# Optimization experiments

Measured on AMD Instinct MI355X. Metric: run time of the kernel, lower is better.

The kernel has to match this reference:

```python
import math
import jax, jax.numpy as jnp
import numpy as np

D_MODEL = 1024
N_HEADS = 16


def setup_inputs() -> dict:
    key = jax.random.key(0)
    ks = jax.random.split(key, 5)
    B, S, D = 4, 2048, D_MODEL
    std = math.sqrt(2.0 / (D + D))
    x = jax.random.normal(ks[0], (B, S, D), dtype=jnp.float32)
    wq = jax.random.normal(ks[1], (D, D), dtype=jnp.float32) * std
    wk = jax.random.normal(ks[2], (D, D), dtype=jnp.float32) * std
    wv = jax.random.normal(ks[3], (D, D), dtype=jnp.float32) * std
    wo = jax.random.normal(ks[4], (D, D), dtype=jnp.float32) * std
    return {"x": x, "wq": wq, "wk": wk, "wv": wv, "wo": wo}


def reference(x, wq, wk, wv, wo):
    B, S, D = x.shape
    H = N_HEADS
    dk = D // H
    # projections: weight is (d_out, d_in) -> y_...j = x_...i W_ji
    def proj(w):
        y = jnp.einsum('bsi,ji->bsj', x, w)
        return y.reshape(B, S, H, dk).transpose(0, 2, 1, 3)  # b h s dk
    Q, K, V = proj(wq), proj(wk), proj(wv)
    scores = jnp.einsum('bhnd,bhmd->bhnm', Q, K) / math.sqrt(dk)
    causal = jnp.tril(jnp.ones((S, S), dtype=bool))  # True = attend
    scores = jnp.where(causal, scores, -jnp.inf)
    weights = jax.nn.softmax(scores, axis=-1)
    attn = jnp.einsum('bhnm,bhmd->bhnd', weights, V)
    attn = attn.transpose(0, 2, 1, 3).reshape(B, S, D)
    return jnp.einsum('bsi,ji->bsj', attn, wo)
```

## Files before the change

### kernel.cpp

```cpp
#include <hip/hip_runtime.h>
#include <hip/hip_bf16.h>
#include <cstdint>

#define D_MODEL 1024
#define NHEADS  16
#define DK      64
#define BATCH   4
#define SEQ     2048
#define MROWS   (BATCH * SEQ)
#define NQT2    (SEQ / 128)
#define NW_ELEM (D_MODEL * D_MODEL)

#define QSCALE 0.18033688011112042f

typedef __attribute__((ext_vector_type(4))) float  f32x4;
typedef __attribute__((ext_vector_type(8))) __bf16 bf16x8;
typedef __attribute__((ext_vector_type(8))) short  short8;

__device__ __forceinline__ unsigned short f2bf(float f) {
    unsigned int u = __float_as_uint(f);
    unsigned int r = (u + 0x7fffu + ((u >> 16) & 1u)) >> 16;
    return (unsigned short)r;
}

__device__ __forceinline__ unsigned int cvtpk_bf16(float lo, float hi) {
    unsigned int r;
    asm volatile("v_cvt_pk_bf16_f32 %0, %1, %2" : "=v"(r) : "v"(lo), "v"(hi));
    return r;
}

__device__ __forceinline__ float exp2_raw(float x) {
    float r;
    asm("v_exp_f32 %0, %1" : "=v"(r) : "v"(x));
    return r;
}

__device__ __forceinline__ void permlane32_swap(unsigned int& a, unsigned int& b) {
    asm("v_permlane32_swap_b32 %0, %1" : "+v"(a), "+v"(b));
}
__device__ __forceinline__ void permlane16_swap(unsigned int& a, unsigned int& b) {
    asm("v_permlane16_swap_b32 %0, %1" : "+v"(a), "+v"(b));
}

__global__ void cvt_bf16(const float* __restrict__ in, unsigned short* __restrict__ out, int n) {
    int i = (blockIdx.x * 256 + threadIdx.x) * 4;
    if (i >= n) return;
    float4 v = *reinterpret_cast<const float4*>(in + i);
    ushort4 o;
    o.x = f2bf(v.x); o.y = f2bf(v.y); o.z = f2bf(v.z); o.w = f2bf(v.w);
    *reinterpret_cast<ushort4*>(out + i) = o;
}

__global__ void cvt_bf16_w(const float* __restrict__ w0, const float* __restrict__ w1,
                           const float* __restrict__ w2, const float* __restrict__ w3,
                           unsigned short* __restrict__ o0, unsigned short* __restrict__ o1,
                           unsigned short* __restrict__ o2, unsigned short* __restrict__ o3,
                           int n) {
    const int z = blockIdx.y;
    const float* in = (z == 0) ? w0 : (z == 1) ? w1 : (z == 2) ? w2 : w3;
    unsigned short* out = (z == 0) ? o0 : (z == 1) ? o1 : (z == 2) ? o2 : o3;
    int i = (blockIdx.x * 256 + threadIdx.x) * 4;
    if (i >= n) return;
    float4 v = *reinterpret_cast<const float4*>(in + i);
    ushort4 o;
    o.x = f2bf(v.x); o.y = f2bf(v.y); o.z = f2bf(v.z); o.w = f2bf(v.w);
    *reinterpret_cast<ushort4*>(out + i) = o;
}

__device__ __forceinline__ void gload_lds16(const void* g, void* l) {
    __builtin_amdgcn_global_load_lds(
        (const __attribute__((address_space(1))) void*)(uintptr_t)g,
        (__attribute__((address_space(3))) void*)(unsigned int)(uintptr_t)l,
        16, 0, 0);
}

#define BM 128
#define BN 128
#define BK 32

__global__ __launch_bounds__(256, 2) void gemm_qkv(
    const unsigned short* __restrict__ A,
    const unsigned short* __restrict__ W,
    unsigned short* __restrict__ Cq,
    unsigned short* __restrict__ Ck,
    unsigned short* __restrict__ Cv)
{
    __shared__ __align__(16) unsigned short As[2][BM * BK];
    __shared__ __align__(16) unsigned short Bs[3][2][BN * BK];

    const int K = D_MODEL, N = D_MODEL;
    const int tid  = threadIdx.x;
    const int wave = tid >> 6;
    const int lane = tid & 63;
    const int wr   = wave >> 1;
    const int wc   = wave & 1;
    const int bm   = blockIdx.x * BM;
    const int bn   = blockIdx.y * BN;

    f32x4 acc[3][4][4];
    #pragma unroll
    for (int w = 0; w < 3; w++)
        #pragma unroll
        for (int i = 0; i < 4; i++)
            #pragma unroll
            for (int j = 0; j < 4; j++)
                #pragma unroll
                for (int r = 0; r < 4; r++) acc[w][i][j][r] = 0.f;

    const int srow = tid >> 2;
    const int scol = (tid & 3) * 8;

    const int kg = (lane >> 4) * 8;
    const int rl = lane & 15;

    const unsigned short* Arow0 = A + (size_t)(bm + srow) * K + scol;
    const unsigned short* Arow1 = A + (size_t)(bm + 64 + srow) * K + scol;
    const unsigned short* Wrow0 = W + (size_t)(bn + srow) * K + scol;
    const unsigned short* Wrow1 = W + (size_t)(bn + 64 + srow) * K + scol;

    auto STAGE = [&](int buf, int k0) {
        gload_lds16(Arow0 + k0, &As[buf][0] + wave * 512);
        gload_lds16(Arow1 + k0, &As[buf][0] + 2048 + wave * 512);
        #pragma unroll
        for (int w = 0; w < 3; w++) {
            gload_lds16(Wrow0 + (size_t)w * NW_ELEM + k0, &Bs[w][buf][0] + wave * 512);
            gload_lds16(Wrow1 + (size_t)w * NW_ELEM + k0, &Bs[w][buf][0] + 2048 + wave * 512);
        }
    };

    auto COMPUTE = [&](int buf) {
        bf16x8 a[4];
        #pragma unroll
        for (int mi = 0; mi < 4; mi++) {
            short8 t = *reinterpret_cast<const short8*>(&As[buf][(wr * 64 + mi * 16 + rl) * BK + kg]);
            a[mi] = __builtin_bit_cast(bf16x8, t);
        }
        #pragma unroll
        for (int w = 0; w < 3; w++)
            #pragma unroll
            for (int ni = 0; ni < 4; ni++) {
                short8 t = *reinterpret_cast<const short8*>(&Bs[w][buf][(wc * 64 + ni * 16 + rl) * BK + kg]);
                bf16x8 b = __builtin_bit_cast(bf16x8, t);
                #pragma unroll
                for (int mi = 0; mi < 4; mi++)
                    acc[w][mi][ni] = __builtin_amdgcn_mfma_f32_16x16x32_bf16(a[mi], b, acc[w][mi][ni], 0, 0, 0);
            }
    };

    const int NT = K / BK;

    STAGE(0, 0);
    __syncthreads();

    int cur = 0;
    for (int t = 0; t < NT - 1; ++t) {
        STAGE(cur ^ 1, (t + 1) * BK);
        COMPUTE(cur);
        __syncthreads();
        cur ^= 1;
    }
    COMPUTE(cur);

    const int rg = (lane >> 4) * 4;
    #pragma unroll
    for (int w = 0; w < 3; w++) {
        unsigned short* C = (w == 0) ? Cq : (w == 1) ? Ck : Cv;
        const float cs = (w == 0) ? QSCALE : 1.0f;
        #pragma unroll
        for (int mi = 0; mi < 4; mi++)
            #pragma unroll
            for (int ni = 0; ni < 4; ni++)
                #pragma unroll
                for (int r = 0; r < 4; r++) {
                    int row = bm + wr * 64 + mi * 16 + rg + r;
                    int col = bn + wc * 64 + ni * 16 + rl;
                    C[(size_t)row * N + col] = f2bf(acc[w][mi][ni][r] * cs);
                }
    }
}

__global__ __launch_bounds__(256) void gemm_out(
    const unsigned short* __restrict__ A,
    const unsigned short* __restrict__ Bt,
    float* __restrict__ C)
{
    __shared__ __align__(16) unsigned short As[2][BM * BK];
    __shared__ __align__(16) unsigned short Bs[2][BN * BK];

    const int K = D_MODEL, N = D_MODEL;
    const int tid  = threadIdx.x;
    const int wave = tid >> 6;
    const int lane = tid & 63;
    const int wr   = wave >> 1;
    const int wc   = wave & 1;
    const int bm   = blockIdx.x * BM;
    const int bn   = blockIdx.y * BN;

    f32x4 acc[4][4];
    #pragma unroll
    for (int i = 0; i < 4; i++)
        #pragma unroll
        for (int j = 0; j < 4; j++)
            #pragma unroll
            for (int r = 0; r < 4; r++) acc[i][j][r] = 0.f;

    const int srow = tid >> 2;
    const int scol = (tid & 3) * 8;

    const int kg = (lane >> 4) * 8;
    const int rl = lane & 15;

    const unsigned short* Arow0 = A  + (size_t)(bm + srow) * K + scol;
    const unsigned short* Arow1 = A  + (size_t)(bm + 64 + srow) * K + scol;
    const unsigned short* Brow0 = Bt + (size_t)(bn + srow) * K + scol;
    const unsigned short* Brow1 = Bt + (size_t)(bn + 64 + srow) * K + scol;

    auto STAGE = [&](int buf, int k0) {
        gload_lds16(Arow0 + k0, &As[buf][0] + wave * 512);
        gload_lds16(Arow1 + k0, &As[buf][0] + 2048 + wave * 512);
        gload_lds16(Brow0 + k0, &Bs[buf][0] + wave * 512);
        gload_lds16(Brow1 + k0, &Bs[buf][0] + 2048 + wave * 512);
    };

    auto COMPUTE = [&](int buf) {
        bf16x8 a[4], b[4];
        #pragma unroll
        for (int mi = 0; mi < 4; mi++) {
            short8 t = *reinterpret_cast<const short8*>(&As[buf][(wr * 64 + mi * 16 + rl) * BK + kg]);
            a[mi] = __builtin_bit_cast(bf16x8, t);
        }
        #pragma unroll
        for (int ni = 0; ni < 4; ni++) {
            short8 t = *reinterpret_cast<const short8*>(&Bs[buf][(wc * 64 + ni * 16 + rl) * BK + kg]);
            b[ni] = __builtin_bit_cast(bf16x8, t);
        }
        #pragma unroll
        for (int mi = 0; mi < 4; mi++)
            #pragma unroll
            for (int ni = 0; ni < 4; ni++)
                acc[mi][ni] = __builtin_amdgcn_mfma_f32_16x16x32_bf16(a[mi], b[ni], acc[mi][ni], 0, 0, 0);
    };

    const int NT = K / BK;

    STAGE(0, 0);
    __syncthreads();

    int cur = 0;
    for (int t = 0; t < NT - 1; ++t) {
        STAGE(cur ^ 1, (t + 1) * BK);
        COMPUTE(cur);
        __syncthreads();
        cur ^= 1;
    }
    COMPUTE(cur);

    const int rg = (lane >> 4) * 4;
    #pragma unroll
    for (int mi = 0; mi < 4; mi++)
        #pragma unroll
        for (int ni = 0; ni < 4; ni++)
            #pragma unroll
            for (int r = 0; r < 4; r++) {
                int row = bm + wr * 64 + mi * 16 + rg + r;
                int col = bn + wc * 64 + ni * 16 + rl;
                C[(size_t)row * N + col] = acc[mi][ni][r];
            }
}

__global__ __launch_bounds__(512, 4) void attn_mfma(
    const unsigned short* __restrict__ Q,
    const unsigned short* __restrict__ K,
    const unsigned short* __restrict__ V,
    unsigned short* __restrict__ O)
{
    __shared__ __align__(16) unsigned short Ks[2][64 * 64];
    __shared__ __align__(16) unsigned short Vt[2][64 * 64];

    const int bh  = blockIdx.x;
    const int b   = bh >> 4;
    const int h   = bh & 15;
    const int qt  = NQT2 - 1 - blockIdx.y;
    const int tid = threadIdx.x;
    const int wave = tid >> 6;
    const int lane = tid & 63;
    const int lg   = lane >> 4;
    const int lq   = lane & 15;

    const size_t base = ((size_t)b * SEQ) * D_MODEL + h * DK;
    const unsigned short* Kb = K + base;
    const unsigned short* Vb = V + base;

    const int qw  = qt * 128 + wave * 16;
    const int myq = qw + lq;

    bf16x8 qf[2];
    {
        const unsigned short* qp = Q + base + (size_t)myq * D_MODEL + lg * 8;
        qf[0] = __builtin_bit_cast(bf16x8, *reinterpret_cast<const short8*>(qp));
        qf[1] = __builtin_bit_cast(bf16x8, *reinterpret_cast<const short8*>(qp + 32));
    }

    const short8 ones_s = {(short)0x3F80, (short)0x3F80, (short)0x3F80, (short)0x3F80,
                           (short)0x3F80, (short)0x3F80, (short)0x3F80, (short)0x3F80};
    const bf16x8 onesf = __builtin_bit_cast(bf16x8, ones_s);

    f32x4 acc[4];
    f32x4 acc_l;
    #pragma unroll
    for (int i = 0; i < 4; i++)
        #pragma unroll
        for (int r = 0; r < 4; r++) acc[i][r] = 0.f;
    #pragma unroll
    for (int r = 0; r < 4; r++) acc_l[r] = 0.f;

    const int trow  = tid >> 3;
    const int tslot = tid & 7;
    const unsigned short* Ksrc = Kb + (size_t)trow * D_MODEL + (tslot ^ (trow & 7)) * 8;

    const unsigned short* Vsrc = Vb + (size_t)lane * D_MODEL + wave * 8;
    union { uint4 v; unsigned short u[8]; } vpre;

    const int nt = 2 * qt + 2;

    gload_lds16(Ksrc, &Ks[0][0] + wave * 512);
    vpre.v = *reinterpret_cast<const uint4*>(Vsrc);
    #pragma unroll
    for (int e = 0; e < 8; ++e) {
        const int addr = (wave * 8 + e) * 128 + ((lane * 2) ^ (e << 4));
        *reinterpret_cast<unsigned short*>((char*)&Vt[0][0] + addr) = vpre.u[e];
    }
    __syncthreads();

    for (int t = 0; t < nt; ++t) {
        const int c = t & 1;
        const bool pf = (t + 1 < nt);

        if (pf) {
            const size_t moff = (size_t)(t + 1) * 64 * D_MODEL;
            gload_lds16(Ksrc + moff, &Ks[c ^ 1][0] + wave * 512);
            vpre.v = *reinterpret_cast<const uint4*>(Vsrc + moff);
        }

        const int m0 = t * 64;

        if (m0 <= qw + 15) {
            f32x4 s[4];
            __builtin_amdgcn_s_setprio(1);
            #pragma unroll
            for (int kg = 0; kg < 4; ++kg) {
                #pragma unroll
                for (int r = 0; r < 4; ++r) s[kg][r] = 0.f;
                #pragma unroll
                for (int ks = 0; ks < 2; ++ks) {
                    const int row  = kg * 16 + lq;
                    const int slot = (ks * 4 + lg) ^ (row & 7);
                    bf16x8 kf = __builtin_bit_cast(bf16x8,
                        *reinterpret_cast<const short8*>((const char*)&Ks[c][0] + row * 128 + slot * 16));
                    s[kg] = __builtin_amdgcn_mfma_f32_16x16x32_bf16(kf, qf[ks], s[kg], 0, 0, 0);
                }
            }
            __builtin_amdgcn_s_setprio(0);

            if (m0 + 63 > qw) {
                #pragma unroll
                for (int kg = 0; kg < 4; ++kg)
                    #pragma unroll
                    for (int r = 0; r < 4; ++r)
                        if (m0 + kg * 16 + lg * 4 + r > myq) s[kg][r] = -INFINITY;
            }

            #pragma unroll
            for (int kg = 0; kg < 4; ++kg)
                #pragma unroll
                for (int r = 0; r < 4; ++r)
                    s[kg][r] = exp2_raw(s[kg][r]);

            #pragma unroll
            for (int ks = 0; ks < 2; ++ks) {
                unsigned int A0 = cvtpk_bf16(s[2*ks][0],   s[2*ks][1]);
                unsigned int A1 = cvtpk_bf16(s[2*ks][2],   s[2*ks][3]);
                unsigned int B0 = cvtpk_bf16(s[2*ks+1][0], s[2*ks+1][1]);
                unsigned int B1 = cvtpk_bf16(s[2*ks+1][2], s[2*ks+1][3]);
                permlane32_swap(A0, B0);
                permlane16_swap(A0, B0);
                permlane32_swap(A1, B1);
                permlane16_swap(A1, B1);
                uint4 awv = make_uint4(A0, A1, B0, B1);
                bf16x8 af = __builtin_bit_cast(bf16x8, awv);
                __builtin_amdgcn_s_setprio(1);
                #pragma unroll
                for (int dg = 0; dg < 4; ++dg) {
                    const int d = dg * 16 + lq;
                    const int addr = d * 128 + ((ks * 64 + lg * 16) ^ ((d & 7) << 4));
                    bf16x8 vf = __builtin_bit_cast(bf16x8,
                        *reinterpret_cast<const short8*>((const char*)&Vt[c][0] + addr));
                    acc[dg] = __builtin_amdgcn_mfma_f32_16x16x32_bf16(af, vf, acc[dg], 0, 0, 0);
                }
                acc_l = __builtin_amdgcn_mfma_f32_16x16x32_bf16(af, onesf, acc_l, 0, 0, 0);
                __builtin_amdgcn_s_setprio(0);
            }
        }

        if (pf) {
            #pragma unroll
            for (int e = 0; e < 8; ++e) {
                const int addr = (wave * 8 + e) * 128 + ((lane * 2) ^ (e << 4));
                *reinterpret_cast<unsigned short*>((char*)&Vt[c ^ 1][0] + addr) = vpre.u[e];
            }
        }
        __syncthreads();
    }

    float lv[4];
    #pragma unroll
    for (int r = 0; r < 4; ++r) lv[r] = 1.0f / acc_l[r];
    #pragma unroll
    for (int dg = 0; dg < 4; ++dg)
        #pragma unroll
        for (int r = 0; r < 4; ++r) {
            const int qrow = qw + lg * 4 + r;
            O[base + (size_t)qrow * D_MODEL + dg * 16 + lq] = f2bf(acc[dg][r] * lv[r]);
        }
}

extern "C" void kernel_launch(void* const* d_in, const int* in_sizes, int n_in,
                              void* d_out, int out_size, void* d_ws, size_t ws_size,
                              hipStream_t stream) {
    const float* x  = (const float*)d_in[0];
    const float* wq = (const float*)d_in[1];
    const float* wk = (const float*)d_in[2];
    const float* wv = (const float*)d_in[3];
    const float* wo = (const float*)d_in[4];

    char* ws = (char*)d_ws;
    const size_t NXB = (size_t)MROWS * D_MODEL * 2;
    const size_t NWB = (size_t)D_MODEL * D_MODEL * 2;

    unsigned short* xb  = (unsigned short*)(ws);
    unsigned short* wqb = (unsigned short*)(ws + NXB);
    unsigned short* wkb = (unsigned short*)(ws + NXB + NWB);
    unsigned short* wvb = (unsigned short*)(ws + NXB + 2 * NWB);
    unsigned short* wob = (unsigned short*)(ws + NXB + 3 * NWB);
    unsigned short* Qb  = (unsigned short*)(ws + NXB + 4 * NWB);
    unsigned short* Kb  = (unsigned short*)(ws + NXB + 4 * NWB + NXB);
    unsigned short* Vb  = (unsigned short*)(ws + NXB + 4 * NWB + 2 * NXB);
    unsigned short* Ab  = (unsigned short*)(ws + NXB + 4 * NWB + 3 * NXB);

    const int NX = MROWS * D_MODEL;
    const int NW = D_MODEL * D_MODEL;

    cvt_bf16<<<NX / 1024, 256, 0, stream>>>(x, xb, NX);
    dim3 gw(NW / 1024, 4, 1);
    cvt_bf16_w<<<gw, 256, 0, stream>>>(wq, wk, wv, wo, wqb, wkb, wvb, wob, NW);

    dim3 gqkv(MROWS / BM, D_MODEL / BN, 1);
    gemm_qkv<<<gqkv, 256, 0, stream>>>(xb, wqb, Qb, Kb, Vb);

    dim3 gattn(BATCH * NHEADS, NQT2, 1);
    attn_mfma<<<gattn, 512, 0, stream>>>(Qb, Kb, Vb, Ab);

    dim3 gout(MROWS / BM, D_MODEL / BN, 1);
    gemm_out<<<gout, 256, 0, stream>>>(Ab, wob, (float*)d_out);
}
```

Baseline: 157.0 us.

## Remap GEMM grids to 1D N-fastest order and vectorize V transpose stores

The QKV and output GEMMs now launch a flat 512-block grid where consecutive blocks walk the N tiles of one M row-block. Co-scheduled blocks therefore share the same A tile in cache instead of striding across M. In the attention kernel, the V-to-LDS transpose changes from eight scalar 16-bit stores per thread to 32-bit global loads of two columns across four rows. These are repacked into two 64-bit LDS writes, cutting LDS store instruction count. The grid change hardcodes 512 = (MROWS/BM)*(D/BN), which assumes BM=BN=128.

After: 152.1 us. 1.03x faster.

```diff
diff --git a/kernel.cpp b/kernel.cpp
--- a/kernel.cpp
+++ b/kernel.cpp
@@ -94,8 +94,8 @@
     const int lane = tid & 63;
     const int wr   = wave >> 1;
     const int wc   = wave & 1;
-    const int bm   = blockIdx.x * BM;
-    const int bn   = blockIdx.y * BN;
+    const int bm   = (blockIdx.x >> 3) * BM;
+    const int bn   = (blockIdx.x & 7) * BN;
 
     f32x4 acc[3][4][4];
     #pragma unroll
@@ -193,8 +193,8 @@
     const int lane = tid & 63;
     const int wr   = wave >> 1;
     const int wc   = wave & 1;
-    const int bm   = blockIdx.x * BM;
-    const int bn   = blockIdx.y * BN;
+    const int bm   = (blockIdx.x >> 3) * BM;
+    const int bn   = (blockIdx.x & 7) * BN;
 
     f32x4 acc[4][4];
     #pragma unroll
@@ -318,18 +318,30 @@
     const int tslot = tid & 7;
     const unsigned short* Ksrc = Kb + (size_t)trow * D_MODEL + (tslot ^ (trow & 7)) * 8;
 
-    const unsigned short* Vsrc = Vb + (size_t)lane * D_MODEL + wave * 8;
-    union { uint4 v; unsigned short u[8]; } vpre;
+    const int vg  = tid >> 5;
+    const int vd0 = (tid & 31) * 2;
+    const unsigned short* Vsrc = Vb + (size_t)(4 * vg) * D_MODEL + vd0;
+    unsigned int vpre[4];
+
+    const int va0 = vd0 * 128 + ((vg * 8) ^ ((vd0 & 7) << 4));
+    const int va1 = (vd0 + 1) * 128 + ((vg * 8) ^ (((vd0 + 1) & 7) << 4));
+
+    auto VWRITE = [&](int buf) {
+        unsigned int lo01 = (vpre[0] & 0xffffu) | (vpre[1] << 16);
+        unsigned int lo23 = (vpre[2] & 0xffffu) | (vpre[3] << 16);
+        unsigned int hi01 = (vpre[0] >> 16) | (vpre[1] & 0xffff0000u);
+        unsigned int hi23 = (vpre[2] >> 16) | (vpre[3] & 0xffff0000u);
+        *reinterpret_cast<uint2*>((char*)&Vt[buf][0] + va0) = make_uint2(lo01, lo23);
+        *reinterpret_cast<uint2*>((char*)&Vt[buf][0] + va1) = make_uint2(hi01, hi23);
+    };
 
     const int nt = 2 * qt + 2;
 
     gload_lds16(Ksrc, &Ks[0][0] + wave * 512);
-    vpre.v = *reinterpret_cast<const uint4*>(Vsrc);
-    #pragma unroll
-    for (int e = 0; e < 8; ++e) {
-        const int addr = (wave * 8 + e) * 128 + ((lane * 2) ^ (e << 4));
-        *reinterpret_cast<unsigned short*>((char*)&Vt[0][0] + addr) = vpre.u[e];
-    }
+    #pragma unroll
+    for (int k = 0; k < 4; ++k)
+        vpre[k] = *reinterpret_cast<const unsigned int*>(Vsrc + (size_t)k * D_MODEL);
+    VWRITE(0);
     __syncthreads();
 
     for (int t = 0; t < nt; ++t) {
@@ -339,7 +351,9 @@
         if (pf) {
             const size_t moff = (size_t)(t + 1) * 64 * D_MODEL;
             gload_lds16(Ksrc + moff, &Ks[c ^ 1][0] + wave * 512);
-            vpre.v = *reinterpret_cast<const uint4*>(Vsrc + moff);
+            #pragma unroll
+            for (int k = 0; k < 4; ++k)
+                vpre[k] = *reinterpret_cast<const unsigned int*>(Vsrc + moff + (size_t)k * D_MODEL);
         }
 
         const int m0 = t * 64;
@@ -402,13 +416,7 @@
             }
         }
 
-        if (pf) {
-            #pragma unroll
-            for (int e = 0; e < 8; ++e) {
-                const int addr = (wave * 8 + e) * 128 + ((lane * 2) ^ (e << 4));
-                *reinterpret_cast<unsigned short*>((char*)&Vt[c ^ 1][0] + addr) = vpre.u[e];
-            }
-        }
+        if (pf) VWRITE(c ^ 1);
         __syncthreads();
     }
 
@@ -454,12 +462,10 @@
     dim3 gw(NW / 1024, 4, 1);
     cvt_bf16_w<<<gw, 256, 0, stream>>>(wq, wk, wv, wo, wqb, wkb, wvb, wob, NW);
 
-    dim3 gqkv(MROWS / BM, D_MODEL / BN, 1);
-    gemm_qkv<<<gqkv, 256, 0, stream>>>(xb, wqb, Qb, Kb, Vb);
+    gemm_qkv<<<512, 256, 0, stream>>>(xb, wqb, Qb, Kb, Vb);
 
     dim3 gattn(BATCH * NHEADS, NQT2, 1);
     attn_mfma<<<gattn, 512, 0, stream>>>(Qb, Kb, Vb, Ab);
 
-    dim3 gout(MROWS / BM, D_MODEL / BN, 1);
-    gemm_out<<<gout, 256, 0, stream>>>(Ab, wob, (float*)d_out);
-}
+    gemm_out<<<512, 256, 0, stream>>>(Ab, wob, (float*)d_out);
+}
```
